# Kernel tuning notes

Measured on AMD Instinct MI355X. Metric: run time of the kernel, lower is better.

## Reference

```python
import jax, jax.numpy as jnp
import numpy as np
import math


def _per_component_log_likelihood(x, MU, A, D, PI):
    # x: [N,d]; MU,D: [K,d]; A: [K,d,l]; PI: [K]
    K, d, l = A.shape
    iD = D ** (-2.0)                                   # [K,d]  (1/sigma^2 per feature)
    B = iD[:, :, None] * A                             # [K,d,l] = diag(iD_k) @ A_k
    # L_k = I_l + A_k^T diag(iD_k) A_k  (Woodbury inner matrix)
    L = jnp.eye(l, dtype=x.dtype)[None] + jnp.einsum('kdl,kdm->klm', A, B)
    iL = jnp.linalg.inv(L)                             # [K,l,l]
    # Mahalanobis term m_d[n,k] = xc^T iD xc - (xc^T iD A) iL (A^T iD xc),
    # expanded so we never materialize the [K,N,d] centered tensor.
    t_quad = (x * x) @ iD.T                            # [N,K]
    t_cross = x @ (iD * MU).T                          # [N,K]
    t_const = jnp.sum(iD * MU * MU, axis=1)            # [K]
    term1 = t_quad - 2.0 * t_cross + t_const[None, :]
    y = jnp.einsum('nd,kdl->nkl', x, B) - jnp.einsum('kd,kdl->kl', MU, B)[None]
    term2 = jnp.einsum('nkl,klm,nkm->nk', y, iL, y)
    m_d = term1 - term2                                # [N,K]
    # log|Sigma_k| = log|L_k| - sum_d log iD[k,d]
    log_det_Sigma = jnp.log(jnp.linalg.det(L)) + jnp.sum(jnp.log(D ** 2.0), axis=1)
    log_prob = -0.5 * ((d * math.log(2.0 * math.pi) + log_det_Sigma)[None, :] + m_d)
    # NOTE: faithful to the source, which adds PI (not log PI) here.
    return PI[None, :] + log_prob                      # [N,K]


def setup_inputs() -> dict:
    key = jax.random.key(0)
    k1, k2, k3, k4 = jax.random.split(key, 4)
    N, K, d, l = 500000, 32, 128, 4
    x = jax.random.normal(k1, (N, d), dtype=jnp.float32)
    MU = jax.random.normal(k2, (K, d), dtype=jnp.float32)
    A = 0.1 * jax.random.normal(k3, (K, d, l), dtype=jnp.float32)
    D = jax.random.uniform(k4, (K, d), dtype=jnp.float32, minval=0.5, maxval=1.5)
    PI = jnp.ones((K,), dtype=jnp.float32) / K
    return {"x": x, "MU": MU, "A": A, "D": D, "PI": PI}


def reference(x, MU, A, D, PI):
    comp_ll = _per_component_log_likelihood(x, MU, A, D, PI)   # [N,K]
    return jax.scipy.special.logsumexp(comp_ll, axis=1)        # [N] = MFA.log_prob(x)
```

## Files before the change

kernel.cpp:

```cpp
#include <hip/hip_runtime.h>
#include <hip/hip_bf16.h>

typedef _Float16 half8  __attribute__((ext_vector_type(8)));
typedef _Float16 half2v __attribute__((ext_vector_type(2)));
typedef float    f32x16 __attribute__((ext_vector_type(16)));

#define KC 32
#define DD 128
#define LL 4
#define NBLK 768
#define WPB 4
#define NSLOT (NBLK*WPB)

__device__ inline half2v pkrtz(float a, float b) {
  return __builtin_bit_cast(half2v, __builtin_amdgcn_cvt_pkrtz(a, b));
}
__device__ inline half2v shx2(half2v v, int d) {
  int i = __builtin_bit_cast(int, v);
  i = __shfl_xor(i, d);
  return __builtin_bit_cast(half2v, i);
}
__device__ inline half2v shl2(half2v v, int src) {
  int i = __builtin_bit_cast(int, v);
  i = __shfl(i, src);
  return __builtin_bit_cast(half2v, i);
}
template <int CTRL>
__device__ inline half2v dpp2(half2v v) {
  int i = __builtin_bit_cast(int, v);
  int r = __builtin_amdgcn_update_dpp(i, i, CTRL, 0xF, 0xF, true);
  return __builtin_bit_cast(half2v, r);
}
__device__ inline half2v pmax2(half2v a, half2v b) {
  half2v r;
  r[0] = a[0] > b[0] ? a[0] : b[0];
  r[1] = a[1] > b[1] ? a[1] : b[1];
  return r;
}
__device__ inline half2v sel8(const half2v* p, int i) {
  half2v a = (i & 1) ? p[1] : p[0];
  half2v b = (i & 1) ? p[3] : p[2];
  half2v c = (i & 1) ? p[5] : p[4];
  half2v d = (i & 1) ? p[7] : p[6];
  half2v e = (i & 2) ? b : a;
  half2v f = (i & 2) ? d : c;
  return (i & 4) ? f : e;
}

__global__ __launch_bounds__(256, 3) void mfa_fused(
    const float* __restrict__ x, const float* __restrict__ MU,
    const float* __restrict__ A, const float* __restrict__ D,
    const float* __restrict__ PI, float* __restrict__ out,
    int N, int ntiles, int iters)
{
  __shared__ int4 sWbuf[3072];
  __shared__ float sMeta[672];
  float* sMetaR = sMeta;
  float* sMetaH = sMeta + 512;
  float* sMetaC = sMeta + 640;

  const int tid = threadIdx.x;
  const int k   = tid >> 3;
  const int sub = tid & 7;
  const int dbase = k*DD + sub*16;

  float idv[16], muv[16];
  {
    float (*sPart)[8][16] = (float (*)[8][16])sWbuf;
    float p[16];
#pragma unroll
    for (int i = 0; i < 16; ++i) p[i] = 0.f;
#pragma unroll
    for (int di = 0; di < 16; ++di) {
      const float Dv = D[dbase + di];
      const float id = 1.0f/(Dv*Dv);
      const float mu = MU[dbase + di];
      idv[di] = id; muv[di] = mu;
      const float4 a4 = *(const float4*)(A + (size_t)(dbase + di)*LL);
      const float a[LL] = {a4.x, a4.y, a4.z, a4.w};
      int s = 0;
#pragma unroll
      for (int l = 0; l < LL; ++l) {
#pragma unroll
        for (int m2 = 0; m2 <= l; ++m2) { p[s] += a[l]*id*a[m2]; ++s; }
        p[10 + l] += mu*id*a[l];
      }
      p[14] += id*mu*mu;
      p[15] += __logf(Dv*Dv);
    }
#pragma unroll
    for (int i = 0; i < 16; ++i) sPart[k][sub][i] = p[i];
  }
  __syncthreads();

  if (tid < KC) {
    float (*sPart)[8][16] = (float (*)[8][16])sWbuf;
    const int kk = tid;
    float p[16];
#pragma unroll
    for (int i = 0; i < 16; ++i) p[i] = 0.f;
    for (int s = 0; s < 8; ++s)
#pragma unroll
      for (int i = 0; i < 16; ++i) p[i] += sPart[kk][s][i];

    float Lm[LL][LL];
    {
      int s = 0;
      for (int l = 0; l < LL; ++l)
        for (int m2 = 0; m2 <= l; ++m2) { Lm[l][m2] = p[s]; ++s; }
    }
    for (int l = 0; l < LL; ++l) Lm[l][l] += 1.0f;
    float cv[LL];
    for (int l = 0; l < LL; ++l) cv[l] = p[10 + l];
    const float t_const  = p[14];
    const float sumlogD2 = p[15];

    float Lo[LL][LL];
    for (int i = 0; i < LL; ++i)
      for (int j = 0; j < LL; ++j) Lo[i][j] = 0.f;
    for (int i = 0; i < LL; ++i) {
      float s = Lm[i][i];
      for (int m2 = 0; m2 < i; ++m2) s -= Lo[i][m2]*Lo[i][m2];
      Lo[i][i] = sqrtf(s);
      for (int j = i + 1; j < LL; ++j) {
        float t = Lm[j][i];
        for (int m2 = 0; m2 < i; ++m2) t -= Lo[j][m2]*Lo[i][m2];
        Lo[j][i] = t / Lo[i][i];
      }
    }
    float Ri[LL][LL];
    for (int i = 0; i < LL; ++i)
      for (int j = 0; j < LL; ++j) Ri[i][j] = 0.f;
    for (int i = 0; i < LL; ++i) {
      Ri[i][i] = 1.0f/Lo[i][i];
      for (int j = 0; j < i; ++j) {
        float s = 0.f;
        for (int m2 = j; m2 < i; ++m2) s += Lo[i][m2]*Ri[m2][j];
        Ri[i][j] = -s / Lo[i][i];
      }
    }
    for (int i = 0; i < LL; ++i)
      for (int j = 0; j < LL; ++j) sMetaR[kk*16 + i*4 + j] = Ri[i][j];
    for (int l = 0; l < LL; ++l) {
      float s = 0.f;
      for (int m2 = 0; m2 <= l; ++m2) s += Ri[l][m2]*cv[m2];
      sMetaH[kk*LL + l] = s;
    }
    float logdetL = 0.f;
    for (int i = 0; i < LL; ++i) logdetL += __logf(Lo[i][i]);
    logdetL *= 2.0f;
    const float dlog2pi = 235.24826473f;
    sMetaC[kk] = PI[kk] - 0.5f*(dlog2pi + logdetL + sumlogD2) - 0.5f*t_const;
  }
  __syncthreads();

  {
    float Rm[LL][LL];
#pragma unroll
    for (int l = 0; l < LL; ++l)
#pragma unroll
      for (int m = 0; m < LL; ++m) Rm[l][m] = sMetaR[k*16 + l*4 + m];
    half8* sW8w = (half8*)sWbuf;
#pragma unroll
    for (int h2 = 0; h2 < 2; ++h2) {
      half8 vq, vr, vz0, vz1, vz2, vz3;
#pragma unroll
      for (int j = 0; j < 8; ++j) {
        const int di = 8*h2 + j;
        const float id = idv[di];
        const float mu = muv[di];
        const float4 a4 = *(const float4*)(A + (size_t)(dbase + di)*LL);
        vq[j] = (_Float16)id;
        vr[j] = (_Float16)(id*mu);
        const float s0 = a4.x*Rm[0][0];
        const float s1 = a4.x*Rm[1][0] + a4.y*Rm[1][1];
        const float s2 = a4.x*Rm[2][0] + a4.y*Rm[2][1] + a4.z*Rm[2][2];
        const float s3 = a4.x*Rm[3][0] + a4.y*Rm[3][1] + a4.z*Rm[3][2]
                       + a4.w*Rm[3][3];
        vz0[j] = (_Float16)(id*s0);
        vz1[j] = (_Float16)(id*s1);
        vz2[j] = (_Float16)(id*s2);
        vz3[j] = (_Float16)(id*s3);
      }
      const int lq = (h2 << 5) | k;
      sW8w[(0*8 + sub)*64 + lq] = vq;
      sW8w[(1*8 + sub)*64 + lq] = vr;
      const int tz = 2 + (k >> 3);
      const int lz = (h2 << 5) | ((k & 7) << 2);
      sW8w[(tz*8 + sub)*64 + lz + 0] = vz0;
      sW8w[(tz*8 + sub)*64 + lz + 1] = vz1;
      sW8w[(tz*8 + sub)*64 + lz + 2] = vz2;
      sW8w[(tz*8 + sub)*64 + lz + 3] = vz3;
    }
  }
  __syncthreads();

  const half8* sW8 = (const half8*)sWbuf;
  const int wv = tid >> 6, lane = tid & 63;
  const int c = lane & 31;
  const int h = lane >> 5;
  const float cc = sMetaC[c];
  float hz[4];
#pragma unroll
  for (int zt = 0; zt < 4; ++zt) hz[zt] = sMetaH[(8*zt + (c >> 2))*4 + (c & 3)];
  const int srcl = (lane & 32) | ((c & 7) << 2) | (c & 3);

  for (int it = 0; it < iters; ++it) {
    const int tile = it*NSLOT + (int)blockIdx.x*WPB + wv;
    if (tile >= ntiles) continue;

    int row = tile*32 + c;
    if (row >= N) row = N - 1;
    const float* xr = x + (size_t)row*DD + h*8;

    f32x16 acc[6];
#pragma unroll
    for (int t = 0; t < 6; ++t)
#pragma unroll
      for (int r = 0; r < 16; ++r) acc[t][r] = 0.f;

#pragma unroll
    for (int half_b = 0; half_b < 2; ++half_b) {
      float4 xv[8];
#pragma unroll
      for (int s = 0; s < 4; ++s) {
        const int ss = half_b*4 + s;
        xv[2*s]     = *(const float4*)(xr + ss*16);
        xv[2*s + 1] = *(const float4*)(xr + ss*16 + 4);
      }
#pragma unroll
      for (int s = 0; s < 4; ++s) {
        const int ss = half_b*4 + s;
        const float4 a = xv[2*s], b = xv[2*s + 1];
        union { half8 v; half2v p[4]; } hx, hx2;
        hx.p[0] = pkrtz(a.x, a.y);
        hx.p[1] = pkrtz(a.z, a.w);
        hx.p[2] = pkrtz(b.x, b.y);
        hx.p[3] = pkrtz(b.z, b.w);
        hx2.v = hx.v * hx.v;
        acc[0] = __builtin_amdgcn_mfma_f32_32x32x16_f16(
            hx2.v, sW8[(0*8 + ss)*64 + lane], acc[0], 0, 0, 0);
#pragma unroll
        for (int t = 1; t < 6; ++t)
          acc[t] = __builtin_amdgcn_mfma_f32_32x32x16_f16(
              hx.v, sW8[(t*8 + ss)*64 + lane], acc[t], 0, 0, 0);
      }
    }

    float vp[16];
#pragma unroll
    for (int r = 0; r < 16; ++r)
      vp[r] = acc[1][r] - 0.5f*acc[0][r] + cc;

    half2v tq[4][8];
#pragma unroll
    for (int zt = 0; zt < 4; ++zt)
#pragma unroll
      for (int i = 0; i < 8; ++i) {
        const float e0 = acc[2 + zt][2*i]     - hz[zt];
        const float e1 = acc[2 + zt][2*i + 1] - hz[zt];
        half2v p = pkrtz(e0*e0, e1*e1);
        p = p + dpp2<0xB1>(p);
        p = p + dpp2<0x4E>(p);
        tq[zt][i] = p;
      }
#pragma unroll
    for (int i = 0; i < 8; ++i) {
      half2v b0 = shl2(tq[0][i], srcl);
      half2v b1 = shl2(tq[1][i], srcl);
      half2v b2 = shl2(tq[2][i], srcl);
      half2v b3 = shl2(tq[3][i], srcl);
      half2v m01 = (c & 8)  ? b1 : b0;
      half2v m23 = (c & 8)  ? b3 : b2;
      half2v st  = (c & 16) ? m23 : m01;
      vp[2*i]     += 0.5f*(float)st[0];
      vp[2*i + 1] += 0.5f*(float)st[1];
    }

    half2v pm[8];
#pragma unroll
    for (int i = 0; i < 8; ++i)
      pm[i] = pkrtz(vp[2*i], vp[2*i + 1]);
#pragma unroll
    for (int i = 0; i < 8; ++i) {
      pm[i] = pmax2(pm[i], dpp2<0xB1>(pm[i]));
      pm[i] = pmax2(pm[i], dpp2<0x4E>(pm[i]));
      pm[i] = pmax2(pm[i], dpp2<0x141>(pm[i]));
      pm[i] = pmax2(pm[i], dpp2<0x140>(pm[i]));
      pm[i] = pmax2(pm[i], shx2(pm[i], 16));
    }

    half2v ps[8];
#pragma unroll
    for (int i = 0; i < 8; ++i) {
      const float e0 = __expf(vp[2*i]     - (float)pm[i][0]);
      const float e1 = __expf(vp[2*i + 1] - (float)pm[i][1]);
      ps[i] = pkrtz(e0, e1);
    }
#pragma unroll
    for (int i = 0; i < 8; ++i) {
      ps[i] = ps[i] + dpp2<0xB1>(ps[i]);
      ps[i] = ps[i] + dpp2<0x4E>(ps[i]);
      ps[i] = ps[i] + dpp2<0x141>(ps[i]);
      ps[i] = ps[i] + dpp2<0x140>(ps[i]);
      ps[i] = ps[i] + shx2(ps[i], 16);
    }

    if (c < 16) {
      const half2v S = sel8(ps, c >> 1);
      const half2v M = sel8(pm, c >> 1);
      const float sum = (c & 1) ? (float)S[1] : (float)S[0];
      const float mx  = (c & 1) ? (float)M[1] : (float)M[0];
      const int rw = tile*32 + (c & 3) + 8*(c >> 2) + 4*h;
      if (rw < N) out[rw] = mx + __logf(sum);
    }
  }
}

extern "C" void kernel_launch(void* const* d_in, const int* in_sizes, int n_in,
                              void* d_out, int out_size, void* d_ws, size_t ws_size,
                              hipStream_t stream) {
  (void)n_in; (void)out_size; (void)d_ws; (void)ws_size;
  const float* x  = (const float*)d_in[0];
  const float* MU = (const float*)d_in[1];
  const float* A  = (const float*)d_in[2];
  const float* D  = (const float*)d_in[3];
  const float* PI = (const float*)d_in[4];
  float* out = (float*)d_out;

  const int N = in_sizes[0] / DD;
  const int ntiles = (N + 31) / 32;
  const int iters  = (ntiles + NSLOT - 1) / NSLOT;
  hipLaunchKernelGGL(mfa_fused, dim3(NBLK), dim3(256), 0, stream,
                     x, MU, A, D, PI, out, N, ntiles, iters);
}
```

Baseline: 370.3 us.

## Software-pipeline x loads across tiles and fold quadratic terms into one accumulator

The x row loads are now software-pipelined: the first half of the next tile's row is prefetched while the current tile's MFMAs run, and the second half is loaded before the first half is consumed. The -0.5 factor is folded into the quadratic weights and a 1/sqrt(2) factor into the Woodbury projection weights and offsets. This lets the squared and linear terms accumulate into a single MFMA accumulator, cutting accumulator registers from six tiles to five and removing some epilogue arithmetic. The trade-offs are higher register pressure from the prefetch buffers, prefetching past the last tile (clamped to row N-1), and slightly different fp16 rounding.

```diff
diff --git a/kernel.cpp b/kernel.cpp
--- a/kernel.cpp
+++ b/kernel.cpp
@@ -161,6 +161,7 @@
 #pragma unroll
       for (int m = 0; m < LL; ++m) Rm[l][m] = sMetaR[k*16 + l*4 + m];
     half8* sW8w = (half8*)sWbuf;
+    const float sc = 0.70710678118654752f;
 #pragma unroll
     for (int h2 = 0; h2 < 2; ++h2) {
       half8 vq, vr, vz0, vz1, vz2, vz3;
@@ -170,17 +171,17 @@
         const float id = idv[di];
         const float mu = muv[di];
         const float4 a4 = *(const float4*)(A + (size_t)(dbase + di)*LL);
-        vq[j] = (_Float16)id;
+        vq[j] = (_Float16)(-0.5f*id);
         vr[j] = (_Float16)(id*mu);
         const float s0 = a4.x*Rm[0][0];
         const float s1 = a4.x*Rm[1][0] + a4.y*Rm[1][1];
         const float s2 = a4.x*Rm[2][0] + a4.y*Rm[2][1] + a4.z*Rm[2][2];
         const float s3 = a4.x*Rm[3][0] + a4.y*Rm[3][1] + a4.z*Rm[3][2]
                        + a4.w*Rm[3][3];
-        vz0[j] = (_Float16)(id*s0);
-        vz1[j] = (_Float16)(id*s1);
-        vz2[j] = (_Float16)(id*s2);
-        vz3[j] = (_Float16)(id*s3);
+        vz0[j] = (_Float16)(sc*id*s0);
+        vz1[j] = (_Float16)(sc*id*s1);
+        vz2[j] = (_Float16)(sc*id*s2);
+        vz3[j] = (_Float16)(sc*id*s3);
       }
       const int lq = (h2 << 5) | k;
       sW8w[(0*8 + sub)*64 + lq] = vq;
@@ -202,63 +203,101 @@
   const float cc = sMetaC[c];
   float hz[4];
 #pragma unroll
-  for (int zt = 0; zt < 4; ++zt) hz[zt] = sMetaH[(8*zt + (c >> 2))*4 + (c & 3)];
+  for (int zt = 0; zt < 4; ++zt)
+    hz[zt] = 0.70710678118654752f * sMetaH[(8*zt + (c >> 2))*4 + (c & 3)];
   const int srcl = (lane & 32) | ((c & 7) << 2) | (c & 3);
 
+  const int tbase = (int)blockIdx.x*WPB + wv;
+  auto rowptr = [&](int it) -> const float* {
+    int row = (it*NSLOT + tbase)*32 + c;
+    if (row >= N) row = N - 1;
+    return x + (size_t)row*DD + h*8;
+  };
+
+  const float* xr = rowptr(0);
+  float4 xvP[8];
+#pragma unroll
+  for (int s = 0; s < 4; ++s) {
+    xvP[2*s]     = *(const float4*)(xr + s*16);
+    xvP[2*s + 1] = *(const float4*)(xr + s*16 + 4);
+  }
+
   for (int it = 0; it < iters; ++it) {
-    const int tile = it*NSLOT + (int)blockIdx.x*WPB + wv;
+    const int tile = it*NSLOT + tbase;
+
+    float4 xvB[8];
+#pragma unroll
+    for (int s = 0; s < 4; ++s) {
+      xvB[2*s]     = *(const float4*)(xr + (4 + s)*16);
+      xvB[2*s + 1] = *(const float4*)(xr + (4 + s)*16 + 4);
+    }
+
+    f32x16 acc[5];
+#pragma unroll
+    for (int t = 0; t < 5; ++t)
+#pragma unroll
+      for (int r = 0; r < 16; ++r) acc[t][r] = 0.f;
+
+#pragma unroll
+    for (int ss = 0; ss < 4; ++ss) {
+      const float4 a = xvP[2*ss], b = xvP[2*ss + 1];
+      union { half8 v; half2v p[4]; } hx, hx2;
+      hx.p[0] = pkrtz(a.x, a.y);
+      hx.p[1] = pkrtz(a.z, a.w);
+      hx.p[2] = pkrtz(b.x, b.y);
+      hx.p[3] = pkrtz(b.z, b.w);
+      hx2.v = hx.v * hx.v;
+      acc[0] = __builtin_amdgcn_mfma_f32_32x32x16_f16(
+          hx2.v, sW8[(0*8 + ss)*64 + lane], acc[0], 0, 0, 0);
+#pragma unroll
+      for (int t = 0; t < 4; ++t)
+        acc[1 + t] = __builtin_amdgcn_mfma_f32_32x32x16_f16(
+            hx.v, sW8[((2 + t)*8 + ss)*64 + lane], acc[1 + t], 0, 0, 0);
+      acc[0] = __builtin_amdgcn_mfma_f32_32x32x16_f16(
+          hx.v, sW8[(1*8 + ss)*64 + lane], acc[0], 0, 0, 0);
+    }
+
+    const float* xrN = rowptr(it + 1);
+#pragma unroll
+    for (int s = 0; s < 4; ++s) {
+      xvP[2*s]     = *(const float4*)(xrN + s*16);
+      xvP[2*s + 1] = *(const float4*)(xrN + s*16 + 4);
+    }
+    xr = xrN;
+
+#pragma unroll
+    for (int ss = 4; ss < 8; ++ss) {
+      const float4 a = xvB[2*(ss - 4)], b = xvB[2*(ss - 4) + 1];
+      union { half8 v; half2v p[4]; } hx, hx2;
+      hx.p[0] = pkrtz(a.x, a.y);
+      hx.p[1] = pkrtz(a.z, a.w);
+      hx.p[2] = pkrtz(b.x, b.y);
+      hx.p[3] = pkrtz(b.z, b.w);
+      hx2.v = hx.v * hx.v;
+      acc[0] = __builtin_amdgcn_mfma_f32_32x32x16_f16(
+          hx2.v, sW8[(0*8 + ss)*64 + lane], acc[0], 0, 0, 0);
+#pragma unroll
+      for (int t = 0; t < 4; ++t)
+        acc[1 + t] = __builtin_amdgcn_mfma_f32_32x32x16_f16(
+            hx.v, sW8[((2 + t)*8 + ss)*64 + lane], acc[1 + t], 0, 0, 0);
+      acc[0] = __builtin_amdgcn_mfma_f32_32x32x16_f16(
+          hx.v, sW8[(1*8 + ss)*64 + lane], acc[0], 0, 0, 0);
+    }
+
     if (tile >= ntiles) continue;
 
-    int row = tile*32 + c;
-    if (row >= N) row = N - 1;
-    const float* xr = x + (size_t)row*DD + h*8;
-
-    f32x16 acc[6];
-#pragma unroll
-    for (int t = 0; t < 6; ++t)
-#pragma unroll
-      for (int r = 0; r < 16; ++r) acc[t][r] = 0.f;
-
-#pragma unroll
-    for (int half_b = 0; half_b < 2; ++half_b) {
-      float4 xv[8];
-#pragma unroll
-      for (int s = 0; s < 4; ++s) {
-        const int ss = half_b*4 + s;
-        xv[2*s]     = *(const float4*)(xr + ss*16);
-        xv[2*s + 1] = *(const float4*)(xr + ss*16 + 4);
-      }
-#pragma unroll
-      for (int s = 0; s < 4; ++s) {
-        const int ss = half_b*4 + s;
-        const float4 a = xv[2*s], b = xv[2*s + 1];
-        union { half8 v; half2v p[4]; } hx, hx2;
-        hx.p[0] = pkrtz(a.x, a.y);
-        hx.p[1] = pkrtz(a.z, a.w);
-        hx.p[2] = pkrtz(b.x, b.y);
-        hx.p[3] = pkrtz(b.z, b.w);
-        hx2.v = hx.v * hx.v;
-        acc[0] = __builtin_amdgcn_mfma_f32_32x32x16_f16(
-            hx2.v, sW8[(0*8 + ss)*64 + lane], acc[0], 0, 0, 0);
-#pragma unroll
-        for (int t = 1; t < 6; ++t)
-          acc[t] = __builtin_amdgcn_mfma_f32_32x32x16_f16(
-              hx.v, sW8[(t*8 + ss)*64 + lane], acc[t], 0, 0, 0);
-      }
-    }
-
     float vp[16];
 #pragma unroll
     for (int r = 0; r < 16; ++r)
-      vp[r] = acc[1][r] - 0.5f*acc[0][r] + cc;
+      vp[r] = acc[0][r] + cc;
 
     half2v tq[4][8];
 #pragma unroll
     for (int zt = 0; zt < 4; ++zt)
 #pragma unroll
       for (int i = 0; i < 8; ++i) {
-        const float e0 = acc[2 + zt][2*i]     - hz[zt];
-        const float e1 = acc[2 + zt][2*i + 1] - hz[zt];
+        const float e0 = acc[1 + zt][2*i]     - hz[zt];
+        const float e1 = acc[1 + zt][2*i + 1] - hz[zt];
         half2v p = pkrtz(e0*e0, e1*e1);
         p = p + dpp2<0xB1>(p);
         p = p + dpp2<0x4E>(p);
@@ -273,8 +312,8 @@
       half2v m01 = (c & 8)  ? b1 : b0;
       half2v m23 = (c & 8)  ? b3 : b2;
       half2v st  = (c & 16) ? m23 : m01;
-      vp[2*i]     += 0.5f*(float)st[0];
-      vp[2*i + 1] += 0.5f*(float)st[1];
+      vp[2*i]     += (float)st[0];
+      vp[2*i + 1] += (float)st[1];
     }
 
     half2v pm[8];
```

Result: slower. 477.0 us (+28.8%).

## Double-buffer x tile loads across iterations and fold quad/cross MFMAs into one accumulator

Applied to the files above, without the earlier changes.

Software-pipelines the persistent loop: the next tile's 128 floats per lane are prefetched into a second register buffer while the current tile's MFMAs and logsumexp run, using a two-step unrolled macro. The quadratic and cross terms now accumulate into a single MFMA accumulator by pre-scaling the diagonal weights by -0.5 and the Woodbury weights by 1/sqrt(2), which drops one accumulator and several VALU ops. Grid size and occupancy are reduced (512 blocks, 2 waves per SIMD bound) to make room for the extra registers. The trade-off is lower occupancy and some redundant prefetch loads past the end, clamped to the last row.

```diff
diff --git a/kernel.cpp b/kernel.cpp
--- a/kernel.cpp
+++ b/kernel.cpp
@@ -8,7 +8,7 @@
 #define KC 32
 #define DD 128
 #define LL 4
-#define NBLK 768
+#define NBLK 512
 #define WPB 4
 #define NSLOT (NBLK*WPB)
 
@@ -47,7 +47,7 @@
   return (i & 4) ? f : e;
 }
 
-__global__ __launch_bounds__(256, 3) void mfa_fused(
+__global__ __launch_bounds__(256, 2) void mfa_fused(
     const float* __restrict__ x, const float* __restrict__ MU,
     const float* __restrict__ A, const float* __restrict__ D,
     const float* __restrict__ PI, float* __restrict__ out,
@@ -161,6 +161,7 @@
 #pragma unroll
       for (int m = 0; m < LL; ++m) Rm[l][m] = sMetaR[k*16 + l*4 + m];
     half8* sW8w = (half8*)sWbuf;
+    const float sc = 0.70710678118654752f;
 #pragma unroll
     for (int h2 = 0; h2 < 2; ++h2) {
       half8 vq, vr, vz0, vz1, vz2, vz3;
@@ -170,17 +171,17 @@
         const float id = idv[di];
         const float mu = muv[di];
         const float4 a4 = *(const float4*)(A + (size_t)(dbase + di)*LL);
-        vq[j] = (_Float16)id;
+        vq[j] = (_Float16)(-0.5f*id);
         vr[j] = (_Float16)(id*mu);
         const float s0 = a4.x*Rm[0][0];
         const float s1 = a4.x*Rm[1][0] + a4.y*Rm[1][1];
         const float s2 = a4.x*Rm[2][0] + a4.y*Rm[2][1] + a4.z*Rm[2][2];
         const float s3 = a4.x*Rm[3][0] + a4.y*Rm[3][1] + a4.z*Rm[3][2]
                        + a4.w*Rm[3][3];
-        vz0[j] = (_Float16)(id*s0);
-        vz1[j] = (_Float16)(id*s1);
-        vz2[j] = (_Float16)(id*s2);
-        vz3[j] = (_Float16)(id*s3);
+        vz0[j] = (_Float16)(sc*id*s0);
+        vz1[j] = (_Float16)(sc*id*s1);
+        vz2[j] = (_Float16)(sc*id*s2);
+        vz3[j] = (_Float16)(sc*id*s3);
       }
       const int lq = (h2 << 5) | k;
       sW8w[(0*8 + sub)*64 + lq] = vq;
@@ -202,119 +203,131 @@
   const float cc = sMetaC[c];
   float hz[4];
 #pragma unroll
-  for (int zt = 0; zt < 4; ++zt) hz[zt] = sMetaH[(8*zt + (c >> 2))*4 + (c & 3)];
+  for (int zt = 0; zt < 4; ++zt)
+    hz[zt] = 0.70710678118654752f * sMetaH[(8*zt + (c >> 2))*4 + (c & 3)];
   const int srcl = (lane & 32) | ((c & 7) << 2) | (c & 3);
-
-  for (int it = 0; it < iters; ++it) {
-    const int tile = it*NSLOT + (int)blockIdx.x*WPB + wv;
-    if (tile >= ntiles) continue;
-
-    int row = tile*32 + c;
-    if (row >= N) row = N - 1;
-    const float* xr = x + (size_t)row*DD + h*8;
-
-    f32x16 acc[6];
-#pragma unroll
-    for (int t = 0; t < 6; ++t)
-#pragma unroll
-      for (int r = 0; r < 16; ++r) acc[t][r] = 0.f;
-
-#pragma unroll
-    for (int half_b = 0; half_b < 2; ++half_b) {
-      float4 xv[8];
-#pragma unroll
-      for (int s = 0; s < 4; ++s) {
-        const int ss = half_b*4 + s;
-        xv[2*s]     = *(const float4*)(xr + ss*16);
-        xv[2*s + 1] = *(const float4*)(xr + ss*16 + 4);
-      }
-#pragma unroll
-      for (int s = 0; s < 4; ++s) {
-        const int ss = half_b*4 + s;
-        const float4 a = xv[2*s], b = xv[2*s + 1];
-        union { half8 v; half2v p[4]; } hx, hx2;
-        hx.p[0] = pkrtz(a.x, a.y);
-        hx.p[1] = pkrtz(a.z, a.w);
-        hx.p[2] = pkrtz(b.x, b.y);
-        hx.p[3] = pkrtz(b.z, b.w);
-        hx2.v = hx.v * hx.v;
-        acc[0] = __builtin_amdgcn_mfma_f32_32x32x16_f16(
-            hx2.v, sW8[(0*8 + ss)*64 + lane], acc[0], 0, 0, 0);
-#pragma unroll
-        for (int t = 1; t < 6; ++t)
-          acc[t] = __builtin_amdgcn_mfma_f32_32x32x16_f16(
-              hx.v, sW8[(t*8 + ss)*64 + lane], acc[t], 0, 0, 0);
-      }
-    }
-
-    float vp[16];
-#pragma unroll
-    for (int r = 0; r < 16; ++r)
-      vp[r] = acc[1][r] - 0.5f*acc[0][r] + cc;
-
-    half2v tq[4][8];
-#pragma unroll
-    for (int zt = 0; zt < 4; ++zt)
-#pragma unroll
-      for (int i = 0; i < 8; ++i) {
-        const float e0 = acc[2 + zt][2*i]     - hz[zt];
-        const float e1 = acc[2 + zt][2*i + 1] - hz[zt];
-        half2v p = pkrtz(e0*e0, e1*e1);
-        p = p + dpp2<0xB1>(p);
-        p = p + dpp2<0x4E>(p);
-        tq[zt][i] = p;
-      }
-#pragma unroll
-    for (int i = 0; i < 8; ++i) {
-      half2v b0 = shl2(tq[0][i], srcl);
-      half2v b1 = shl2(tq[1][i], srcl);
-      half2v b2 = shl2(tq[2][i], srcl);
-      half2v b3 = shl2(tq[3][i], srcl);
-      half2v m01 = (c & 8)  ? b1 : b0;
-      half2v m23 = (c & 8)  ? b3 : b2;
-      half2v st  = (c & 16) ? m23 : m01;
-      vp[2*i]     += 0.5f*(float)st[0];
-      vp[2*i + 1] += 0.5f*(float)st[1];
-    }
-
-    half2v pm[8];
-#pragma unroll
-    for (int i = 0; i < 8; ++i)
-      pm[i] = pkrtz(vp[2*i], vp[2*i + 1]);
-#pragma unroll
-    for (int i = 0; i < 8; ++i) {
-      pm[i] = pmax2(pm[i], dpp2<0xB1>(pm[i]));
-      pm[i] = pmax2(pm[i], dpp2<0x4E>(pm[i]));
-      pm[i] = pmax2(pm[i], dpp2<0x141>(pm[i]));
-      pm[i] = pmax2(pm[i], dpp2<0x140>(pm[i]));
-      pm[i] = pmax2(pm[i], shx2(pm[i], 16));
-    }
-
-    half2v ps[8];
-#pragma unroll
-    for (int i = 0; i < 8; ++i) {
-      const float e0 = __expf(vp[2*i]     - (float)pm[i][0]);
-      const float e1 = __expf(vp[2*i + 1] - (float)pm[i][1]);
-      ps[i] = pkrtz(e0, e1);
-    }
-#pragma unroll
-    for (int i = 0; i < 8; ++i) {
-      ps[i] = ps[i] + dpp2<0xB1>(ps[i]);
-      ps[i] = ps[i] + dpp2<0x4E>(ps[i]);
-      ps[i] = ps[i] + dpp2<0x141>(ps[i]);
-      ps[i] = ps[i] + dpp2<0x140>(ps[i]);
-      ps[i] = ps[i] + shx2(ps[i], 16);
-    }
-
-    if (c < 16) {
-      const half2v S = sel8(ps, c >> 1);
-      const half2v M = sel8(pm, c >> 1);
-      const float sum = (c & 1) ? (float)S[1] : (float)S[0];
-      const float mx  = (c & 1) ? (float)M[1] : (float)M[0];
-      const int rw = tile*32 + (c & 3) + 8*(c >> 2) + 4*h;
-      if (rw < N) out[rw] = mx + __logf(sum);
-    }
-  }
+  const int tbase = (int)blockIdx.x*WPB + wv;
+
+  float4 xA[16], xB[16];
+
+  {
+    int row0 = tbase*32 + c;
+    if (row0 >= N) row0 = N - 1;
+    const float* xr = x + (size_t)row0*DD + h*8;
+#pragma unroll
+    for (int s = 0; s < 8; ++s) {
+      xA[2*s]     = *(const float4*)(xr + s*16);
+      xA[2*s + 1] = *(const float4*)(xr + s*16 + 4);
+    }
+  }
+
+#define STEP(XC, XN, IT)                                                      \
+  {                                                                           \
+    const int tile = (IT)*NSLOT + tbase;                                      \
+     \
+    {                                                                         \
+      int rowN = ((IT) + 1)*NSLOT*32 + tbase*32 + c;                          \
+      if (rowN >= N) rowN = N - 1;                                            \
+      const float* xrN = x + (size_t)rowN*DD + h*8;                           \
+      _Pragma("unroll")                                                       \
+      for (int s = 0; s < 8; ++s) {                                           \
+        XN[2*s]     = *(const float4*)(xrN + s*16);                           \
+        XN[2*s + 1] = *(const float4*)(xrN + s*16 + 4);                       \
+      }                                                                       \
+    }                                                                         \
+    f32x16 acc[5];                                                            \
+    _Pragma("unroll")                                                         \
+    for (int t = 0; t < 5; ++t)                                               \
+      _Pragma("unroll")                                                       \
+      for (int r = 0; r < 16; ++r) acc[t][r] = 0.f;                           \
+    _Pragma("unroll")                                                         \
+    for (int ss = 0; ss < 8; ++ss) {                                          \
+      const float4 a = XC[2*ss], b = XC[2*ss + 1];                            \
+      union { half8 v; half2v p[4]; } hx, hx2;                                \
+      hx.p[0] = pkrtz(a.x, a.y);                                              \
+      hx.p[1] = pkrtz(a.z, a.w);                                              \
+      hx.p[2] = pkrtz(b.x, b.y);                                              \
+      hx.p[3] = pkrtz(b.z, b.w);                                              \
+      hx2.v = hx.v * hx.v;                                                    \
+      acc[0] = __builtin_amdgcn_mfma_f32_32x32x16_f16(                        \
+          hx2.v, sW8[(0*8 + ss)*64 + lane], acc[0], 0, 0, 0);                 \
+      _Pragma("unroll")                                                       \
+      for (int t = 0; t < 4; ++t)                                             \
+        acc[1 + t] = __builtin_amdgcn_mfma_f32_32x32x16_f16(                  \
+            hx.v, sW8[((2 + t)*8 + ss)*64 + lane], acc[1 + t], 0, 0, 0);      \
+      acc[0] = __builtin_amdgcn_mfma_f32_32x32x16_f16(                        \
+          hx.v, sW8[(1*8 + ss)*64 + lane], acc[0], 0, 0, 0);                  \
+    }                                                                         \
+    if (tile < ntiles) {                                                      \
+      float vp[16];                                                           \
+      _Pragma("unroll")                                                       \
+      for (int r = 0; r < 16; ++r) vp[r] = acc[0][r] + cc;                    \
+      half2v tq[4][8];                                                        \
+      _Pragma("unroll")                                                       \
+      for (int zt = 0; zt < 4; ++zt)                                          \
+        _Pragma("unroll")                                                     \
+        for (int i = 0; i < 8; ++i) {                                         \
+          const float e0 = acc[1 + zt][2*i]     - hz[zt];                     \
+          const float e1 = acc[1 + zt][2*i + 1] - hz[zt];                     \
+          half2v p = pkrtz(e0*e0, e1*e1);                                     \
+          p = p + dpp2<0xB1>(p);                                              \
+          p = p + dpp2<0x4E>(p);                                              \
+          tq[zt][i] = p;                                                      \
+        }                                                                     \
+      _Pragma("unroll")                                                       \
+      for (int i = 0; i < 8; ++i) {                                           \
+        half2v b0 = shl2(tq[0][i], srcl);                                     \
+        half2v b1 = shl2(tq[1][i], srcl);                                     \
+        half2v b2 = shl2(tq[2][i], srcl);                                     \
+        half2v b3 = shl2(tq[3][i], srcl);                                     \
+        half2v m01 = (c & 8)  ? b1 : b0;                                      \
+        half2v m23 = (c & 8)  ? b3 : b2;                                      \
+        half2v st  = (c & 16) ? m23 : m01;                                    \
+        vp[2*i]     += (float)st[0];                                          \
+        vp[2*i + 1] += (float)st[1];                                          \
+      }                                                                       \
+      half2v pm[8];                                                           \
+      _Pragma("unroll")                                                       \
+      for (int i = 0; i < 8; ++i) pm[i] = pkrtz(vp[2*i], vp[2*i + 1]);        \
+      _Pragma("unroll")                                                       \
+      for (int i = 0; i < 8; ++i) {                                           \
+        pm[i] = pmax2(pm[i], dpp2<0xB1>(pm[i]));                              \
+        pm[i] = pmax2(pm[i], dpp2<0x4E>(pm[i]));                              \
+        pm[i] = pmax2(pm[i], dpp2<0x141>(pm[i]));                             \
+        pm[i] = pmax2(pm[i], dpp2<0x140>(pm[i]));                             \
+        pm[i] = pmax2(pm[i], shx2(pm[i], 16));                                \
+      }                                                                       \
+      half2v ps[8];                                                           \
+      _Pragma("unroll")                                                       \
+      for (int i = 0; i < 8; ++i) {                                           \
+        const float e0 = __expf(vp[2*i]     - (float)pm[i][0]);               \
+        const float e1 = __expf(vp[2*i + 1] - (float)pm[i][1]);               \
+        ps[i] = pkrtz(e0, e1);                                                \
+      }                                                                       \
+      _Pragma("unroll")                                                       \
+      for (int i = 0; i < 8; ++i) {                                           \
+        ps[i] = ps[i] + dpp2<0xB1>(ps[i]);                                    \
+        ps[i] = ps[i] + dpp2<0x4E>(ps[i]);                                    \
+        ps[i] = ps[i] + dpp2<0x141>(ps[i]);                                   \
+        ps[i] = ps[i] + dpp2<0x140>(ps[i]);                                   \
+        ps[i] = ps[i] + shx2(ps[i], 16);                                      \
+      }                                                                       \
+      if (c < 16) {                                                           \
+        const half2v S = sel8(ps, c >> 1);                                    \
+        const half2v M = sel8(pm, c >> 1);                                    \
+        const float sum = (c & 1) ? (float)S[1] : (float)S[0];                \
+        const float mx  = (c & 1) ? (float)M[1] : (float)M[0];                \
+        const int rw = tile*32 + (c & 3) + 8*(c >> 2) + 4*h;                  \
+        if (rw < N) out[rw] = mx + __logf(sum);                               \
+      }                                                                       \
+    }                                                                         \
+  }
+
+  for (int it = 0; it < iters; it += 2) {
+    STEP(xA, xB, it);
+    STEP(xB, xA, it + 1);
+  }
+#undef STEP
 }
 
 extern "C" void kernel_launch(void* const* d_in, const int* in_sizes, int n_in,
```

Result: no change. 370.0 us (-0.1%).

## Stage x through LDS with async double-buffered loads and restructure MFMA operands

Applied to the files above, without the earlier changes.

Replaces direct global loads of x with global_load_lds async copies into a per-wave double-buffered, XOR-swizzled LDS stage, using explicit vmcnt waits so loads for the next slice overlap the MFMAs of the current one. The quadratic and cross terms are folded into one accumulator by keeping the -0.5*iD and iD*MU fragments in registers. The Woodbury z-projections are laid out per component and pre-scaled by 1/sqrt(2), so the quadratic correction becomes a per-lane square-accumulate, dropping the DPP and shuffle reduction. Grid and occupancy drop to 512 blocks at 2 waves per SIMD to fit the larger LDS footprint. Out-of-range and idle lanes now write to a workspace dummy, which relies on the workspace being large enough.

```diff
diff --git a/kernel.cpp b/kernel.cpp
--- a/kernel.cpp
+++ b/kernel.cpp
@@ -8,7 +8,7 @@
 #define KC 32
 #define DD 128
 #define LL 4
-#define NBLK 768
+#define NBLK 512
 #define WPB 4
 #define NSLOT (NBLK*WPB)
 
@@ -18,11 +18,6 @@
 __device__ inline half2v shx2(half2v v, int d) {
   int i = __builtin_bit_cast(int, v);
   i = __shfl_xor(i, d);
-  return __builtin_bit_cast(half2v, i);
-}
-__device__ inline half2v shl2(half2v v, int src) {
-  int i = __builtin_bit_cast(int, v);
-  i = __shfl(i, src);
   return __builtin_bit_cast(half2v, i);
 }
 template <int CTRL>
@@ -46,15 +41,28 @@
   half2v f = (i & 2) ? d : c;
   return (i & 4) ? f : e;
 }
-
-__global__ __launch_bounds__(256, 3) void mfa_fused(
+__device__ inline void stage16(const float* g, float* l) {
+  __builtin_amdgcn_global_load_lds(
+      (const __attribute__((address_space(1))) void*)g,
+      (__attribute__((address_space(3))) void*)l, 16, 0, 0);
+}
+__device__ inline float4 lds_read16(const float* p) {
+  float4 d;
+  unsigned a = (unsigned)(unsigned long long)
+      (const __attribute__((address_space(3))) float*)p;
+  asm volatile("ds_read_b128 %0, %1" : "=v"(d) : "v"(a));
+  return d;
+}
+
+__global__ __launch_bounds__(256, 2) void mfa_fused(
     const float* __restrict__ x, const float* __restrict__ MU,
     const float* __restrict__ A, const float* __restrict__ D,
     const float* __restrict__ PI, float* __restrict__ out,
-    int N, int ntiles, int iters)
+    float* __restrict__ dws, int N, int ntiles, int iters)
 {
-  __shared__ int4 sWbuf[3072];
-  __shared__ float sMeta[672];
+  __shared__ half8 sWz[2048];
+  __shared__ float sStage[8192];
+  float* sMeta  = sStage + 4096;
   float* sMetaR = sMeta;
   float* sMetaH = sMeta + 512;
   float* sMetaC = sMeta + 640;
@@ -64,9 +72,8 @@
   const int sub = tid & 7;
   const int dbase = k*DD + sub*16;
 
-  float idv[16], muv[16];
   {
-    float (*sPart)[8][16] = (float (*)[8][16])sWbuf;
+    float (*sPart)[8][16] = (float (*)[8][16])sStage;
     float p[16];
 #pragma unroll
     for (int i = 0; i < 16; ++i) p[i] = 0.f;
@@ -75,7 +82,6 @@
       const float Dv = D[dbase + di];
       const float id = 1.0f/(Dv*Dv);
       const float mu = MU[dbase + di];
-      idv[di] = id; muv[di] = mu;
       const float4 a4 = *(const float4*)(A + (size_t)(dbase + di)*LL);
       const float a[LL] = {a4.x, a4.y, a4.z, a4.w};
       int s = 0;
@@ -94,7 +100,7 @@
   __syncthreads();
 
   if (tid < KC) {
-    float (*sPart)[8][16] = (float (*)[8][16])sWbuf;
+    float (*sPart)[8][16] = (float (*)[8][16])sStage;
     const int kk = tid;
     float p[16];
 #pragma unroll
@@ -160,127 +166,148 @@
     for (int l = 0; l < LL; ++l)
 #pragma unroll
       for (int m = 0; m < LL; ++m) Rm[l][m] = sMetaR[k*16 + l*4 + m];
-    half8* sW8w = (half8*)sWbuf;
+    const float sc = 0.70710678118654752f;
 #pragma unroll
     for (int h2 = 0; h2 < 2; ++h2) {
-      half8 vq, vr, vz0, vz1, vz2, vz3;
+      half8 vz0, vz1, vz2, vz3;
 #pragma unroll
       for (int j = 0; j < 8; ++j) {
         const int di = 8*h2 + j;
-        const float id = idv[di];
-        const float mu = muv[di];
+        const float Dv = D[dbase + di];
+        const float id = 1.0f/(Dv*Dv);
         const float4 a4 = *(const float4*)(A + (size_t)(dbase + di)*LL);
-        vq[j] = (_Float16)id;
-        vr[j] = (_Float16)(id*mu);
         const float s0 = a4.x*Rm[0][0];
         const float s1 = a4.x*Rm[1][0] + a4.y*Rm[1][1];
         const float s2 = a4.x*Rm[2][0] + a4.y*Rm[2][1] + a4.z*Rm[2][2];
         const float s3 = a4.x*Rm[3][0] + a4.y*Rm[3][1] + a4.z*Rm[3][2]
                        + a4.w*Rm[3][3];
-        vz0[j] = (_Float16)(id*s0);
-        vz1[j] = (_Float16)(id*s1);
-        vz2[j] = (_Float16)(id*s2);
-        vz3[j] = (_Float16)(id*s3);
-      }
-      const int lq = (h2 << 5) | k;
-      sW8w[(0*8 + sub)*64 + lq] = vq;
-      sW8w[(1*8 + sub)*64 + lq] = vr;
-      const int tz = 2 + (k >> 3);
-      const int lz = (h2 << 5) | ((k & 7) << 2);
-      sW8w[(tz*8 + sub)*64 + lz + 0] = vz0;
-      sW8w[(tz*8 + sub)*64 + lz + 1] = vz1;
-      sW8w[(tz*8 + sub)*64 + lz + 2] = vz2;
-      sW8w[(tz*8 + sub)*64 + lz + 3] = vz3;
-    }
-  }
-  __syncthreads();
-
-  const half8* sW8 = (const half8*)sWbuf;
+        vz0[j] = (_Float16)(sc*id*s0);
+        vz1[j] = (_Float16)(sc*id*s1);
+        vz2[j] = (_Float16)(sc*id*s2);
+        vz3[j] = (_Float16)(sc*id*s3);
+      }
+      const int lp = (h2 << 5) | k;
+      sWz[(0*8 + sub)*64 + lp] = vz0;
+      sWz[(1*8 + sub)*64 + lp] = vz1;
+      sWz[(2*8 + sub)*64 + lp] = vz2;
+      sWz[(3*8 + sub)*64 + lp] = vz3;
+    }
+  }
+
   const int wv = tid >> 6, lane = tid & 63;
   const int c = lane & 31;
   const int h = lane >> 5;
+  const int sw7 = c & 7;
   const float cc = sMetaC[c];
   float hz[4];
 #pragma unroll
-  for (int zt = 0; zt < 4; ++zt) hz[zt] = sMetaH[(8*zt + (c >> 2))*4 + (c & 3)];
-  const int srcl = (lane & 32) | ((c & 7) << 2) | (c & 3);
+  for (int zt = 0; zt < 4; ++zt)
+    hz[zt] = 0.70710678118654752f * sMetaH[c*4 + zt];
+
+  half8 qf[8], rf[8];
+#pragma unroll
+  for (int ss = 0; ss < 8; ++ss) {
+    const float* dp = D  + (size_t)c*DD + ss*16 + h*8;
+    const float* mp = MU + (size_t)c*DD + ss*16 + h*8;
+    const float4 d0 = *(const float4*)dp, d1 = *(const float4*)(dp + 4);
+    const float4 m0 = *(const float4*)mp, m1 = *(const float4*)(mp + 4);
+    const float i0 = 1.f/(d0.x*d0.x), i1 = 1.f/(d0.y*d0.y);
+    const float i2 = 1.f/(d0.z*d0.z), i3 = 1.f/(d0.w*d0.w);
+    const float i4 = 1.f/(d1.x*d1.x), i5 = 1.f/(d1.y*d1.y);
+    const float i6 = 1.f/(d1.z*d1.z), i7 = 1.f/(d1.w*d1.w);
+    union { half8 v; half2v p[4]; } q, r;
+    q.p[0] = pkrtz(-0.5f*i0, -0.5f*i1);
+    q.p[1] = pkrtz(-0.5f*i2, -0.5f*i3);
+    q.p[2] = pkrtz(-0.5f*i4, -0.5f*i5);
+    q.p[3] = pkrtz(-0.5f*i6, -0.5f*i7);
+    r.p[0] = pkrtz(i0*m0.x, i1*m0.y);
+    r.p[1] = pkrtz(i2*m0.z, i3*m0.w);
+    r.p[2] = pkrtz(i4*m1.x, i5*m1.y);
+    r.p[3] = pkrtz(i6*m1.z, i7*m1.w);
+    qf[ss] = q.v; rf[ss] = r.v;
+  }
+  __syncthreads();
+
+  const int tbase = (int)blockIdx.x*WPB + wv;
+  const int gid   = (int)blockIdx.x*256 + tid;
+
+  auto stageF = [&](int itS, int slS) {
+    const int trow = (itS*NSLOT + tbase)*32;
+    float* lb = sStage + wv*2048 + (slS & 1)*1024;
+#pragma unroll
+    for (int m = 0; m < 4; ++m) {
+      int r0 = trow + m*8 + (lane >> 3);
+      if (r0 >= N) r0 = N - 1;
+      const float* src = x + (size_t)r0*DD + slS*32
+                       + 4*((lane & 7) ^ ((lane >> 3) & 7));
+      stage16(src, lb + m*256);
+    }
+  };
+
+#define MM(SS, XA, XB)                                                        \
+  {                                                                           \
+    union { half8 v; half2v p[4]; } hx, hx2;                                  \
+    hx.p[0] = pkrtz((XA).x, (XA).y);                                          \
+    hx.p[1] = pkrtz((XA).z, (XA).w);                                          \
+    hx.p[2] = pkrtz((XB).x, (XB).y);                                          \
+    hx.p[3] = pkrtz((XB).z, (XB).w);                                          \
+    hx2.v = hx.v * hx.v;                                                      \
+    acc[0] = __builtin_amdgcn_mfma_f32_32x32x16_f16(hx2.v, qf[SS], acc[0], 0,0,0); \
+    acc[1] = __builtin_amdgcn_mfma_f32_32x32x16_f16(hx.v, sWz[(0*8+(SS))*64 + lane], acc[1], 0,0,0); \
+    acc[2] = __builtin_amdgcn_mfma_f32_32x32x16_f16(hx.v, sWz[(1*8+(SS))*64 + lane], acc[2], 0,0,0); \
+    acc[3] = __builtin_amdgcn_mfma_f32_32x32x16_f16(hx.v, sWz[(2*8+(SS))*64 + lane], acc[3], 0,0,0); \
+    acc[4] = __builtin_amdgcn_mfma_f32_32x32x16_f16(hx.v, sWz[(3*8+(SS))*64 + lane], acc[4], 0,0,0); \
+    acc[0] = __builtin_amdgcn_mfma_f32_32x32x16_f16(hx.v, rf[SS], acc[0], 0,0,0); \
+  }
+
+#define STEPK(SL, WVMSTR, ITS, SLS)                                           \
+  {                                                                           \
+    asm volatile("s_waitcnt vmcnt(" WVMSTR ")" ::: "memory");                 \
+    __builtin_amdgcn_sched_barrier(0);                                        \
+    const float* sb = sStage + wv*2048 + ((SL) & 1)*1024 + (size_t)c*32;      \
+    const float4 xa0 = lds_read16(sb + (((2*h + 0) ^ sw7) << 2));             \
+    const float4 xa1 = lds_read16(sb + (((2*h + 1) ^ sw7) << 2));             \
+    const float4 xb0 = lds_read16(sb + (((4 + 2*h + 0) ^ sw7) << 2));         \
+    const float4 xb1 = lds_read16(sb + (((4 + 2*h + 1) ^ sw7) << 2));         \
+    asm volatile("s_waitcnt lgkmcnt(0)" ::: "memory");                        \
+    __builtin_amdgcn_sched_barrier(0);                                        \
+    stageF((ITS), (SLS));                                                     \
+    __builtin_amdgcn_sched_barrier(0);                                        \
+    MM((SL)*2 + 0, xa0, xa1);                                                 \
+    MM((SL)*2 + 1, xb0, xb1);                                                 \
+  }
+
+  stageF(0, 0);
+  stageF(0, 1);
+  dws[gid] = 0.f;
+  __builtin_amdgcn_sched_barrier(0);
 
   for (int it = 0; it < iters; ++it) {
-    const int tile = it*NSLOT + (int)blockIdx.x*WPB + wv;
-    if (tile >= ntiles) continue;
-
-    int row = tile*32 + c;
-    if (row >= N) row = N - 1;
-    const float* xr = x + (size_t)row*DD + h*8;
-
-    f32x16 acc[6];
-#pragma unroll
-    for (int t = 0; t < 6; ++t)
+    f32x16 acc[5];
+#pragma unroll
+    for (int t = 0; t < 5; ++t)
 #pragma unroll
       for (int r = 0; r < 16; ++r) acc[t][r] = 0.f;
 
-#pragma unroll
-    for (int half_b = 0; half_b < 2; ++half_b) {
-      float4 xv[8];
-#pragma unroll
-      for (int s = 0; s < 4; ++s) {
-        const int ss = half_b*4 + s;
-        xv[2*s]     = *(const float4*)(xr + ss*16);
-        xv[2*s + 1] = *(const float4*)(xr + ss*16 + 4);
-      }
-#pragma unroll
-      for (int s = 0; s < 4; ++s) {
-        const int ss = half_b*4 + s;
-        const float4 a = xv[2*s], b = xv[2*s + 1];
-        union { half8 v; half2v p[4]; } hx, hx2;
-        hx.p[0] = pkrtz(a.x, a.y);
-        hx.p[1] = pkrtz(a.z, a.w);
-        hx.p[2] = pkrtz(b.x, b.y);
-        hx.p[3] = pkrtz(b.z, b.w);
-        hx2.v = hx.v * hx.v;
-        acc[0] = __builtin_amdgcn_mfma_f32_32x32x16_f16(
-            hx2.v, sW8[(0*8 + ss)*64 + lane], acc[0], 0, 0, 0);
-#pragma unroll
-        for (int t = 1; t < 6; ++t)
-          acc[t] = __builtin_amdgcn_mfma_f32_32x32x16_f16(
-              hx.v, sW8[(t*8 + ss)*64 + lane], acc[t], 0, 0, 0);
-      }
-    }
+    STEPK(0, "5", it,     2)
+    STEPK(1, "5", it,     3)
+    STEPK(2, "4", it + 1, 0)
+    STEPK(3, "4", it + 1, 1)
 
     float vp[16];
 #pragma unroll
-    for (int r = 0; r < 16; ++r)
-      vp[r] = acc[1][r] - 0.5f*acc[0][r] + cc;
-
-    half2v tq[4][8];
+    for (int r = 0; r < 16; ++r) vp[r] = acc[0][r] + cc;
 #pragma unroll
     for (int zt = 0; zt < 4; ++zt)
 #pragma unroll
-      for (int i = 0; i < 8; ++i) {
-        const float e0 = acc[2 + zt][2*i]     - hz[zt];
-        const float e1 = acc[2 + zt][2*i + 1] - hz[zt];
-        half2v p = pkrtz(e0*e0, e1*e1);
-        p = p + dpp2<0xB1>(p);
-        p = p + dpp2<0x4E>(p);
-        tq[zt][i] = p;
-      }
-#pragma unroll
-    for (int i = 0; i < 8; ++i) {
-      half2v b0 = shl2(tq[0][i], srcl);
-      half2v b1 = shl2(tq[1][i], srcl);
-      half2v b2 = shl2(tq[2][i], srcl);
-      half2v b3 = shl2(tq[3][i], srcl);
-      half2v m01 = (c & 8)  ? b1 : b0;
-      half2v m23 = (c & 8)  ? b3 : b2;
-      half2v st  = (c & 16) ? m23 : m01;
-      vp[2*i]     += 0.5f*(float)st[0];
-      vp[2*i + 1] += 0.5f*(float)st[1];
-    }
+      for (int r = 0; r < 16; ++r) {
+        const float e = acc[1 + zt][r] - hz[zt];
+        vp[r] += e*e;
+      }
 
     half2v pm[8];
 #pragma unroll
-    for (int i = 0; i < 8; ++i)
-      pm[i] = pkrtz(vp[2*i], vp[2*i + 1]);
+    for (int i = 0; i < 8; ++i) pm[i] = pkrtz(vp[2*i], vp[2*i + 1]);
 #pragma unroll
     for (int i = 0; i < 8; ++i) {
       pm[i] = pmax2(pm[i], dpp2<0xB1>(pm[i]));
@@ -289,7 +316,6 @@
       pm[i] = pmax2(pm[i], dpp2<0x140>(pm[i]));
       pm[i] = pmax2(pm[i], shx2(pm[i], 16));
     }
-
     half2v ps[8];
 #pragma unroll
     for (int i = 0; i < 8; ++i) {
@@ -306,31 +332,35 @@
       ps[i] = ps[i] + shx2(ps[i], 16);
     }
 
-    if (c < 16) {
-      const half2v S = sel8(ps, c >> 1);
-      const half2v M = sel8(pm, c >> 1);
-      const float sum = (c & 1) ? (float)S[1] : (float)S[0];
-      const float mx  = (c & 1) ? (float)M[1] : (float)M[0];
-      const int rw = tile*32 + (c & 3) + 8*(c >> 2) + 4*h;
-      if (rw < N) out[rw] = mx + __logf(sum);
-    }
-  }
+    const int tile = it*NSLOT + tbase;
+    const half2v S = sel8(ps, (c & 15) >> 1);
+    const half2v M = sel8(pm, (c & 15) >> 1);
+    const float sum = (c & 1) ? (float)S[1] : (float)S[0];
+    const float mx  = (c & 1) ? (float)M[1] : (float)M[0];
+    const int rw = tile*32 + (c & 3) + 8*((c & 15) >> 2) + 4*h;
+    const bool valid = (tile < ntiles) && (c < 16) && (rw < N);
+    float* dst = valid ? (out + rw) : (dws + gid);
+    *dst = mx + __logf(sum);
+  }
+#undef STEPK
+#undef MM
 }
 
 extern "C" void kernel_launch(void* const* d_in, const int* in_sizes, int n_in,
                               void* d_out, int out_size, void* d_ws, size_t ws_size,
                               hipStream_t stream) {
-  (void)n_in; (void)out_size; (void)d_ws; (void)ws_size;
+  (void)n_in; (void)out_size; (void)ws_size;
   const float* x  = (const float*)d_in[0];
   const float* MU = (const float*)d_in[1];
   const float* A  = (const float*)d_in[2];
   const float* D  = (const float*)d_in[3];
   const float* PI = (const float*)d_in[4];
   float* out = (float*)d_out;
+  float* dws = (float*)d_ws;
 
   const int N = in_sizes[0] / DD;
   const int ntiles = (N + 31) / 32;
   const int iters  = (ntiles + NSLOT - 1) / NSLOT;
   hipLaunchKernelGGL(mfa_fused, dim3(NBLK), dim3(256), 0, stream,
-                     x, MU, A, D, PI, out, N, ntiles, iters);
-}
+                     x, MU, A, D, PI, out, dws, N, ntiles, iters);
+}
```

Measured after the change: 371.8 us. No clear change (+0.4%).
